# Optimization experiments

Hardware: AMD Instinct MI355X
Metric: run time of the kernel (lower is better)

The kernel has to match this reference:

```python
import jax, jax.numpy as jnp
import numpy as np

TS = 1.0  # simulation time step (Ts from network.yaml)


def alpha_psp(x, tau):
    """SLAYER psp: causal temporal conv of x (time-major, (T,...)) with the
    SRM alpha kernel eps[k] = (k*Ts/tau)*exp(1 - k*Ts/tau), scaled by Ts.
    eps[k] = (Ts*e/tau) * k * d**k with d = exp(-Ts/tau), realized exactly by a
    2-state linear recurrence instead of an O(T^2) FIR."""
    d = jnp.asarray(np.exp(-TS / tau), x.dtype)
    c = jnp.asarray(np.e * TS / tau * TS, x.dtype)  # kernel amp * Ts integration

    def step(carry, x_t):
        u, v = carry                       # u = sum x_s d^(t-1-s); v = sum x_s (t-1-s) d^(t-1-s)
        v_new = d * (v + u)                # -> sum_{s<=t} x_s (t-s) d^(t-s)  (x_t weight 0)
        u_new = d * u + x_t
        return (u_new, v_new), c * v_new

    z = jnp.zeros_like(x[0])
    _, out = jax.lax.scan(step, (z, z), x)
    return out


def lif_spike(u_in, theta, tauRef, scaleRef):
    """SLAYER spike function: sequential threshold over time with alpha-shaped
    refractory response nu[k] = -scaleRef*theta*(k*Ts/tauRef)*exp(1-k*Ts/tauRef)
    added after every spike. Same 2-state recurrence generates the refractory
    sum exactly. u_in is time-major (T, ...). Spike amplitude is 1/Ts."""
    d = jnp.asarray(np.exp(-TS / tauRef), u_in.dtype)
    c = jnp.asarray(-scaleRef * theta * np.e * TS / tauRef, u_in.dtype)

    def step(carry, u_t):
        u, v = carry
        v_new = d * (v + u)                # refractory state from past spikes only
        m = u_t + c * v_new                # membrane potential incl. refractory
        s = (m >= theta).astype(u_t.dtype)
        return (d * u + s, v_new), (s / TS, m)

    z = jnp.zeros_like(u_in[0])
    _, (spikes, membrane) = jax.lax.scan(step, (z, z), u_in)
    return spikes, membrane


def conv2d_t(x, w, pad):
    """Per-time-step 2D conv (SLAYER conv3d with time-kernel 1, no bias).
    x: (T, N, C, H, W), w: (O, I, kh, kw)."""
    T, N, C, H, W = x.shape
    y = jax.lax.conv_general_dilated(
        x.reshape(T * N, C, H, W), w, (1, 1), [(pad, pad), (pad, pad)],
        dimension_numbers=('NCHW', 'OIHW', 'NCHW'))
    return y.reshape(T, N, -1, H, W)


def setup_inputs() -> dict:
    key = jax.random.key(0)
    k1, k2, k3 = jax.random.split(key, 3)
    # binary event spike train, (N, C, H, W, T)
    spikeInput = (jax.random.uniform(k1, (4, 1, 192, 192, 64)) < 0.2).astype(jnp.float32)
    # SLAYER conv weights (bias=False); scaled up (weightScale~100 in SLAYER)
    W1 = jax.random.normal(k2, (1, 1, 5, 5), jnp.float32) * 10.0
    W2 = jax.random.normal(k3, (1, 1, 3, 3), jnp.float32) * 10.0
    return {"spikeInput": spikeInput, "W1": W1, "W2": W2}


def reference(spikeInput, W1, W2):
    x = jnp.moveaxis(spikeInput, -1, 0)          # (T, N, C, H, W) time-major
    psp1 = alpha_psp(x, tau=1.0)                 # slayer1.psp (tauSr=1)
    s1, _ = lif_spike(conv2d_t(psp1, W1, 2), theta=30.0, tauRef=1.0, scaleRef=1.0)
    psp2 = alpha_psp(s1, tau=2.0)                # slayer2.psp (tauSr=2)
    s2, _ = lif_spike(conv2d_t(psp2, W2, 1), theta=50.0, tauRef=2.0, scaleRef=1.0)
    return jnp.moveaxis(s2, 0, -1)               # back to (N, C, H, W, T)
```

## Files before the change

### kernel.cpp

```cpp
#include <hip/hip_runtime.h>


#define HH   192
#define WW   192
#define NIMG 4
#define TT   64
#define TILE 16
#define NT   256
#define XW   6
#define XH   12

#define E_D 2.718281828459045
static constexpr float D1  = (float)0.36787944117144233;
static constexpr float CP1 = (float)(E_D);
static constexpr float DR1 = (float)0.36787944117144233;
static constexpr float CR1 = (float)(-30.0 * E_D);
static constexpr float D2  = (float)0.6065306597126334;
static constexpr float CP2 = (float)(E_D * 0.5);
static constexpr float DR2 = (float)0.6065306597126334;
static constexpr float CR2 = (float)(-50.0 * E_D * 0.5);
static constexpr float TH1 = 30.0f;
static constexpr float TH2 = 50.0f;

__global__ __launch_bounds__(NT)
void ka_pack(const float* __restrict__ in, unsigned* __restrict__ bitT) {
    const int gw = blockIdx.x * (NT / 64) + (threadIdx.x >> 6);
    const int ln = threadIdx.x & 63;
    const int xw = gw % XW;
    const int ny = gw / XW;
    const float* src = in + ((size_t)ny * WW + xw * 32) * TT + ln;
    unsigned w = 0u;
#pragma unroll
    for (int x = 0; x < 32; x++) {
        const float v = src[(size_t)x * TT];
        w |= (v != 0.f) ? (1u << x) : 0u;
    }
    bitT[((size_t)ny * XW + xw) * TT + ln] = w;
}

__global__ __launch_bounds__(NT, 1)
void kb_layer1(const unsigned* __restrict__ bitT, const float* __restrict__ w1g,
               unsigned short* __restrict__ s1h) {
    __shared__ __align__(16) float ct[NT * 65];
    __shared__ float lut[5 * 32];

    const int n = blockIdx.z, ty = blockIdx.y, tx = blockIdx.x;
    const int y0 = ty * TILE, x0 = tx * TILE;
    const int tid = threadIdx.x;
    const int wv = tid >> 6, ln = tid & 63;

    if (tid < 160) {
        const int r = tid >> 5, p = tid & 31;
        float s = 0.f;
#pragma unroll
        for (int j = 0; j < 5; j++)
            if ((p >> j) & 1) s += w1g[r * 5 + j];
        lut[tid] = s;
    }

    const int a = (x0 - 2) >> 5;
    const int s = (x0 - 2) & 31;
    unsigned w20[8];
#pragma unroll
    for (int rr = 0; rr < 8; rr++) {
        const int gy = y0 - 2 + wv * 4 + rr;
        unsigned wa = 0u, wb = 0u;
        if (gy >= 0 && gy < HH) {
            const unsigned* rp = bitT + ((size_t)(n * HH + gy) * XW) * TT + ln;
            if (a >= 0)     wa = rp[(size_t)a * TT];
            if (a + 1 < XW) wb = rp[(size_t)(a + 1) * TT];
        }
        w20[rr] = (wa >> s) | (wb << (32 - s));
    }
    __syncthreads();

#pragma unroll
    for (int rp = 0; rp < 4; rp++) {
        const int row = wv * 4 + rp;
#pragma unroll
        for (int col = 0; col < 16; col++) {
            const float c =
                ((lut[  0 + ((w20[rp + 0] >> col) & 31)]
                + lut[ 32 + ((w20[rp + 1] >> col) & 31)])
                + (lut[ 64 + ((w20[rp + 2] >> col) & 31)]
                +  lut[ 96 + ((w20[rp + 3] >> col) & 31)]))
                +  lut[128 + ((w20[rp + 4] >> col) & 31)];
            ct[(row * 16 + col) * 65 + ln] = c;
        }
    }
    __syncthreads();

    unsigned slo = 0u, shi = 0u;
    {
        const int px = tid;
        float u1 = 0.f, v1 = 0.f, ur = 0.f, vr = 0.f;
#pragma unroll
        for (int tc = 0; tc < TT; tc += 8) {
            float c8[8];
#pragma unroll
            for (int j = 0; j < 8; j++) c8[j] = ct[px * 65 + tc + j];
#pragma unroll
            for (int j = 0; j < 8; j++) {
                v1 = D1 * (v1 + u1);
                const float p = CP1 * v1;
                u1 = D1 * u1 + c8[j];
                vr = DR1 * (vr + ur);
                const float m = p + CR1 * vr;
                const bool sp = (m >= TH1);
                ur = DR1 * ur + (sp ? 1.f : 0.f);
                const unsigned bit = sp ? (1u << ((tc + j) & 31)) : 0u;
                if (tc < 32) slo |= bit;
                else         shi |= bit;
            }
        }
    }
    __syncthreads();
    ((uint2*)ct)[tid] = make_uint2(slo, shi);
    __syncthreads();

    const uint2* tb = (const uint2*)ct;
#pragma unroll
    for (int rp = 0; rp < 4; rp++) {
        const int yl = wv * 4 + rp;
        unsigned h = 0u;
#pragma unroll
        for (int x = 0; x < 16; x++) {
            const uint2 b = tb[yl * 16 + x];
            const unsigned w = (ln < 32) ? b.x : b.y;
            h |= ((w >> (ln & 31)) & 1u) << x;
        }
        s1h[((size_t)(n * HH + y0 + yl) * XH + tx) * TT + ln] = (unsigned short)h;
    }
}

__global__ __launch_bounds__(NT, 1)
void kc_layer2(const unsigned short* __restrict__ s1h, const float* __restrict__ w2g,
               float* __restrict__ out) {
    __shared__ __align__(16) float ct[NT * 65];
    __shared__ float lut[3 * 8];

    const int n = blockIdx.z, ty = blockIdx.y, tx = blockIdx.x;
    const int y0 = ty * TILE, x0 = tx * TILE;
    const int tid = threadIdx.x;
    const int wv = tid >> 6, ln = tid & 63;

    if (tid < 24) {
        const int r = tid >> 3, p = tid & 7;
        float s = 0.f;
#pragma unroll
        for (int j = 0; j < 3; j++)
            if ((p >> j) & 1) s += w2g[r * 3 + j];
        lut[tid] = s;
    }

    unsigned w18[6];
#pragma unroll
    for (int rr = 0; rr < 6; rr++) {
        const int gy = y0 - 1 + wv * 4 + rr;
        unsigned hm = 0u, h0 = 0u, hp = 0u;
        if (gy >= 0 && gy < HH) {
            const unsigned short* rp = s1h + ((size_t)(n * HH + gy) * XH) * TT + ln;
            if (tx > 0)      hm = rp[(size_t)(tx - 1) * TT];
            h0 = rp[(size_t)tx * TT];
            if (tx + 1 < XH) hp = rp[(size_t)(tx + 1) * TT];
        }
        w18[rr] = (hm >> 15) | (h0 << 1) | ((hp & 1u) << 17);
    }
    __syncthreads();

#pragma unroll
    for (int rp = 0; rp < 4; rp++) {
        const int row = wv * 4 + rp;
#pragma unroll
        for (int col = 0; col < 16; col++) {
            const float c =
                (lut[ 0 + ((w18[rp + 0] >> col) & 7)]
               + lut[ 8 + ((w18[rp + 1] >> col) & 7)])
               + lut[16 + ((w18[rp + 2] >> col) & 7)];
            ct[(row * 16 + col) * 65 + ln] = c;
        }
    }
    __syncthreads();

    unsigned olo = 0u, ohi = 0u;
    {
        const int px = tid;
        float u2 = 0.f, v2 = 0.f, ur2 = 0.f, vr2 = 0.f;
#pragma unroll
        for (int tc = 0; tc < TT; tc += 8) {
            float c8[8];
#pragma unroll
            for (int j = 0; j < 8; j++) c8[j] = ct[px * 65 + tc + j];
#pragma unroll
            for (int j = 0; j < 8; j++) {
                v2 = D2 * (v2 + u2);
                const float p = CP2 * v2;
                u2 = D2 * u2 + c8[j];
                vr2 = DR2 * (vr2 + ur2);
                const float m = p + CR2 * vr2;
                const bool sp = (m >= TH2);
                ur2 = DR2 * ur2 + (sp ? 1.f : 0.f);
                const unsigned bit = sp ? (1u << ((tc + j) & 31)) : 0u;
                if (tc < 32) olo |= bit;
                else         ohi |= bit;
            }
        }
    }
    __syncthreads();
    ((uint2*)ct)[tid] = make_uint2(olo, ohi);
    __syncthreads();

    const uint2* tb = (const uint2*)ct;
    const int sh = ln & 31;
#pragma unroll
    for (int k = 0; k < 64; k++) {
        const int p = wv * 64 + k;
        const uint2 b = tb[p];
        const unsigned w = (ln < 32) ? b.x : b.y;
        out[((size_t)(n * HH + y0 + (p >> 4)) * WW + x0 + (p & 15)) * TT + ln] =
            (float)((w >> sh) & 1u);
    }
}

extern "C" void kernel_launch(void* const* d_in, const int* in_sizes, int n_in,
                              void* d_out, int out_size, void* d_ws, size_t ws_size,
                              hipStream_t stream) {
    const float* in = (const float*)d_in[0];
    const float* w1 = (const float*)d_in[1];
    const float* w2 = (const float*)d_in[2];
    float* out = (float*)d_out;

    char* ws = (char*)d_ws;
    unsigned*       bitT = (unsigned*)ws;
    unsigned short* s1h  = (unsigned short*)(ws + (2u << 20));

    const int ka_blocks = (NIMG * HH * XW) / (NT / 64);
    dim3 tgrid(WW / TILE, HH / TILE, NIMG);
    ka_pack  <<<ka_blocks, NT, 0, stream>>>(in, bitT);
    kb_layer1<<<tgrid, NT, 0, stream>>>(bitT, w1, s1h);
    kc_layer2<<<tgrid, NT, 0, stream>>>(s1h, w2, out);
}
```

Measured before the change: 124.9 us.

## Split fused layer kernels into separate conv and scan kernels via global staging

Splits each fused layer kernel into a convolution kernel that writes per-pixel time series to global memory and a scan kernel that reads them back with vector loads. This drops the large shared-memory transpose buffer, so occupancy can rise. Layer 2 now stores 9-bit neighbourhood patterns and looks them up in a 512-entry table, and the output is written as contiguous float4 per pixel. The cost is about 38MB of extra global write and read traffic for the layer-1 float staging, plus two more kernel launches.

```diff
diff --git a/kernel.cpp b/kernel.cpp
--- a/kernel.cpp
+++ b/kernel.cpp
@@ -5,10 +5,10 @@
 #define WW   192
 #define NIMG 4
 #define TT   64
-#define TILE 16
 #define NT   256
 #define XW   6
 #define XH   12
+#define SPR  12
 
 #define E_D 2.718281828459045
 static constexpr float D1  = (float)0.36787944117144233;
@@ -38,16 +38,13 @@
     bitT[((size_t)ny * XW + xw) * TT + ln] = w;
 }
 
-__global__ __launch_bounds__(NT, 1)
-void kb_layer1(const unsigned* __restrict__ bitT, const float* __restrict__ w1g,
-               unsigned short* __restrict__ s1h) {
-    __shared__ __align__(16) float ct[NT * 65];
+__global__ __launch_bounds__(NT)
+void k1_conv1(const unsigned* __restrict__ bitT, const float* __restrict__ w1g,
+              float* __restrict__ ct1) {
     __shared__ float lut[5 * 32];
-
-    const int n = blockIdx.z, ty = blockIdx.y, tx = blockIdx.x;
-    const int y0 = ty * TILE, x0 = tx * TILE;
+    const int n = blockIdx.z, gy = blockIdx.y * 4 + (threadIdx.x >> 6);
+    const int xs = blockIdx.x, ln = threadIdx.x & 63;
     const int tid = threadIdx.x;
-    const int wv = tid >> 6, ln = tid & 63;
 
     if (tid < 160) {
         const int r = tid >> 5, p = tid & 31;
@@ -58,67 +55,75 @@
         lut[tid] = s;
     }
 
+    const int x0 = xs * 16;
     const int a = (x0 - 2) >> 5;
     const int s = (x0 - 2) & 31;
-    unsigned w20[8];
-#pragma unroll
-    for (int rr = 0; rr < 8; rr++) {
-        const int gy = y0 - 2 + wv * 4 + rr;
+    unsigned w20[5];
+#pragma unroll
+    for (int dy = 0; dy < 5; dy++) {
+        const int yy = gy - 2 + dy;
         unsigned wa = 0u, wb = 0u;
-        if (gy >= 0 && gy < HH) {
-            const unsigned* rp = bitT + ((size_t)(n * HH + gy) * XW) * TT + ln;
+        if (yy >= 0 && yy < HH) {
+            const unsigned* rp = bitT + ((size_t)(n * HH + yy) * XW) * TT + ln;
             if (a >= 0)     wa = rp[(size_t)a * TT];
             if (a + 1 < XW) wb = rp[(size_t)(a + 1) * TT];
         }
-        w20[rr] = (wa >> s) | (wb << (32 - s));
+        w20[dy] = (wa >> s) | (wb << (32 - s));
     }
     __syncthreads();
 
-#pragma unroll
-    for (int rp = 0; rp < 4; rp++) {
-        const int row = wv * 4 + rp;
-#pragma unroll
-        for (int col = 0; col < 16; col++) {
-            const float c =
-                ((lut[  0 + ((w20[rp + 0] >> col) & 31)]
-                + lut[ 32 + ((w20[rp + 1] >> col) & 31)])
-                + (lut[ 64 + ((w20[rp + 2] >> col) & 31)]
-                +  lut[ 96 + ((w20[rp + 3] >> col) & 31)]))
-                +  lut[128 + ((w20[rp + 4] >> col) & 31)];
-            ct[(row * 16 + col) * 65 + ln] = c;
-        }
-    }
+    float* op = ct1 + ((size_t)(n * HH + gy) * SPR + xs) * 16 * TT + ln;
+#pragma unroll
+    for (int col = 0; col < 16; col++) {
+        const float c =
+            ((lut[  0 + ((w20[0] >> col) & 31)]
+            + lut[ 32 + ((w20[1] >> col) & 31)])
+            + (lut[ 64 + ((w20[2] >> col) & 31)]
+            +  lut[ 96 + ((w20[3] >> col) & 31)]))
+            +  lut[128 + ((w20[4] >> col) & 31)];
+        op[(size_t)col * TT] = c;
+    }
+}
+
+__global__ __launch_bounds__(NT, 1)
+void k2_scan1(const float* __restrict__ ct1, unsigned short* __restrict__ s1h) {
+    __shared__ uint2 tb[NT];
+    const int n = blockIdx.z, by = blockIdx.y, bx = blockIdx.x;
+    const int tid = threadIdx.x;
+    const int y = by * 16 + (tid >> 4);
+
+    const float4* p = reinterpret_cast<const float4*>(
+        ct1 + (((size_t)(n * HH + y) * SPR + bx) * 16 + (tid & 15)) * TT);
+    float c[TT];
+#pragma unroll
+    for (int j = 0; j < 16; j++) {
+        const float4 v = p[j];
+        c[4 * j + 0] = v.x; c[4 * j + 1] = v.y;
+        c[4 * j + 2] = v.z; c[4 * j + 3] = v.w;
+    }
+
+    float u1 = 0.f, v1 = 0.f, ur = 0.f, vr = 0.f;
+    unsigned slo = 0u, shi = 0u;
+#pragma unroll
+    for (int tc = 0; tc < TT; tc += 8) {
+#pragma unroll
+        for (int j = 0; j < 8; j++) {
+            v1 = D1 * (v1 + u1);
+            const float pp = CP1 * v1;
+            u1 = D1 * u1 + c[tc + j];
+            vr = DR1 * (vr + ur);
+            const float m = pp + CR1 * vr;
+            const bool sp = (m >= TH1);
+            ur = DR1 * ur + (sp ? 1.f : 0.f);
+            const unsigned bit = sp ? (1u << ((tc + j) & 31)) : 0u;
+            if (tc < 32) slo |= bit;
+            else         shi |= bit;
+        }
+    }
+    tb[tid] = make_uint2(slo, shi);
     __syncthreads();
 
-    unsigned slo = 0u, shi = 0u;
-    {
-        const int px = tid;
-        float u1 = 0.f, v1 = 0.f, ur = 0.f, vr = 0.f;
-#pragma unroll
-        for (int tc = 0; tc < TT; tc += 8) {
-            float c8[8];
-#pragma unroll
-            for (int j = 0; j < 8; j++) c8[j] = ct[px * 65 + tc + j];
-#pragma unroll
-            for (int j = 0; j < 8; j++) {
-                v1 = D1 * (v1 + u1);
-                const float p = CP1 * v1;
-                u1 = D1 * u1 + c8[j];
-                vr = DR1 * (vr + ur);
-                const float m = p + CR1 * vr;
-                const bool sp = (m >= TH1);
-                ur = DR1 * ur + (sp ? 1.f : 0.f);
-                const unsigned bit = sp ? (1u << ((tc + j) & 31)) : 0u;
-                if (tc < 32) slo |= bit;
-                else         shi |= bit;
-            }
-        }
-    }
-    __syncthreads();
-    ((uint2*)ct)[tid] = make_uint2(slo, shi);
-    __syncthreads();
-
-    const uint2* tb = (const uint2*)ct;
+    const int wv = tid >> 6, ln = tid & 63;
 #pragma unroll
     for (int rp = 0; rp < 4; rp++) {
         const int yl = wv * 4 + rp;
@@ -129,96 +134,111 @@
             const unsigned w = (ln < 32) ? b.x : b.y;
             h |= ((w >> (ln & 31)) & 1u) << x;
         }
-        s1h[((size_t)(n * HH + y0 + yl) * XH + tx) * TT + ln] = (unsigned short)h;
-    }
-}
-
-__global__ __launch_bounds__(NT, 1)
-void kc_layer2(const unsigned short* __restrict__ s1h, const float* __restrict__ w2g,
-               float* __restrict__ out) {
-    __shared__ __align__(16) float ct[NT * 65];
-    __shared__ float lut[3 * 8];
-
-    const int n = blockIdx.z, ty = blockIdx.y, tx = blockIdx.x;
-    const int y0 = ty * TILE, x0 = tx * TILE;
-    const int tid = threadIdx.x;
-    const int wv = tid >> 6, ln = tid & 63;
-
-    if (tid < 24) {
-        const int r = tid >> 3, p = tid & 7;
-        float s = 0.f;
-#pragma unroll
-        for (int j = 0; j < 3; j++)
-            if ((p >> j) & 1) s += w2g[r * 3 + j];
-        lut[tid] = s;
-    }
-
-    unsigned w18[6];
-#pragma unroll
-    for (int rr = 0; rr < 6; rr++) {
-        const int gy = y0 - 1 + wv * 4 + rr;
+        s1h[((size_t)(n * HH + by * 16 + yl) * XH + bx) * TT + ln] =
+            (unsigned short)h;
+    }
+}
+
+__global__ __launch_bounds__(NT)
+void k3_conv2(const unsigned short* __restrict__ s1h,
+              unsigned short* __restrict__ ct2p) {
+    const int n = blockIdx.z, gy = blockIdx.y * 4 + (threadIdx.x >> 6);
+    const int tx = blockIdx.x, ln = threadIdx.x & 63;
+
+    unsigned w18[3];
+#pragma unroll
+    for (int dy = 0; dy < 3; dy++) {
+        const int yy = gy - 1 + dy;
         unsigned hm = 0u, h0 = 0u, hp = 0u;
-        if (gy >= 0 && gy < HH) {
-            const unsigned short* rp = s1h + ((size_t)(n * HH + gy) * XH) * TT + ln;
+        if (yy >= 0 && yy < HH) {
+            const unsigned short* rp =
+                s1h + ((size_t)(n * HH + yy) * XH) * TT + ln;
             if (tx > 0)      hm = rp[(size_t)(tx - 1) * TT];
             h0 = rp[(size_t)tx * TT];
             if (tx + 1 < XH) hp = rp[(size_t)(tx + 1) * TT];
         }
-        w18[rr] = (hm >> 15) | (h0 << 1) | ((hp & 1u) << 17);
+        w18[dy] = (hm >> 15) | (h0 << 1) | ((hp & 1u) << 17);
+    }
+
+    unsigned short* op =
+        ct2p + ((size_t)(n * HH + gy) * SPR + tx) * 16 * TT + ln;
+#pragma unroll
+    for (int col = 0; col < 16; col++) {
+        const unsigned pat = ((w18[0] >> col) & 7)
+                           | (((w18[1] >> col) & 7) << 3)
+                           | (((w18[2] >> col) & 7) << 6);
+        op[(size_t)col * TT] = (unsigned short)pat;
+    }
+}
+
+__global__ __launch_bounds__(NT, 1)
+void k4_scan2(const unsigned short* __restrict__ ct2p,
+              const float* __restrict__ w2g, float* __restrict__ out) {
+    __shared__ float lut3[512];
+    const int n = blockIdx.z, by = blockIdx.y, bx = blockIdx.x;
+    const int tid = threadIdx.x;
+
+#pragma unroll
+    for (int e = tid; e < 512; e += NT) {
+        float l0 = 0.f, l1 = 0.f, l2 = 0.f;
+#pragma unroll
+        for (int j = 0; j < 3; j++) {
+            if ((e >> j) & 1)       l0 += w2g[j];
+            if ((e >> (3 + j)) & 1) l1 += w2g[3 + j];
+            if ((e >> (6 + j)) & 1) l2 += w2g[6 + j];
+        }
+        lut3[e] = (l0 + l1) + l2;
     }
     __syncthreads();
 
-#pragma unroll
-    for (int rp = 0; rp < 4; rp++) {
-        const int row = wv * 4 + rp;
-#pragma unroll
-        for (int col = 0; col < 16; col++) {
-            const float c =
-                (lut[ 0 + ((w18[rp + 0] >> col) & 7)]
-               + lut[ 8 + ((w18[rp + 1] >> col) & 7)])
-               + lut[16 + ((w18[rp + 2] >> col) & 7)];
-            ct[(row * 16 + col) * 65 + ln] = c;
-        }
-    }
-    __syncthreads();
-
+    const int y = by * 16 + (tid >> 4), x = bx * 16 + (tid & 15);
+    const uint4* pp = reinterpret_cast<const uint4*>(
+        ct2p + (((size_t)(n * HH + y) * SPR + bx) * 16 + (tid & 15)) * TT);
+    uint4 pr[8];
+#pragma unroll
+    for (int j = 0; j < 8; j++) pr[j] = pp[j];
+
+    float l[TT];
+#pragma unroll
+    for (int j = 0; j < 8; j++) {
+        const unsigned q[4] = {pr[j].x, pr[j].y, pr[j].z, pr[j].w};
+#pragma unroll
+        for (int h = 0; h < 4; h++) {
+            l[j * 8 + 2 * h + 0] = lut3[q[h] & 0x1ffu];
+            l[j * 8 + 2 * h + 1] = lut3[(q[h] >> 16) & 0x1ffu];
+        }
+    }
+
+    float u2 = 0.f, v2 = 0.f, ur2 = 0.f, vr2 = 0.f;
     unsigned olo = 0u, ohi = 0u;
-    {
-        const int px = tid;
-        float u2 = 0.f, v2 = 0.f, ur2 = 0.f, vr2 = 0.f;
-#pragma unroll
-        for (int tc = 0; tc < TT; tc += 8) {
-            float c8[8];
-#pragma unroll
-            for (int j = 0; j < 8; j++) c8[j] = ct[px * 65 + tc + j];
-#pragma unroll
-            for (int j = 0; j < 8; j++) {
-                v2 = D2 * (v2 + u2);
-                const float p = CP2 * v2;
-                u2 = D2 * u2 + c8[j];
-                vr2 = DR2 * (vr2 + ur2);
-                const float m = p + CR2 * vr2;
-                const bool sp = (m >= TH2);
-                ur2 = DR2 * ur2 + (sp ? 1.f : 0.f);
-                const unsigned bit = sp ? (1u << ((tc + j) & 31)) : 0u;
-                if (tc < 32) olo |= bit;
-                else         ohi |= bit;
-            }
-        }
-    }
-    __syncthreads();
-    ((uint2*)ct)[tid] = make_uint2(olo, ohi);
-    __syncthreads();
-
-    const uint2* tb = (const uint2*)ct;
-    const int sh = ln & 31;
-#pragma unroll
-    for (int k = 0; k < 64; k++) {
-        const int p = wv * 64 + k;
-        const uint2 b = tb[p];
-        const unsigned w = (ln < 32) ? b.x : b.y;
-        out[((size_t)(n * HH + y0 + (p >> 4)) * WW + x0 + (p & 15)) * TT + ln] =
-            (float)((w >> sh) & 1u);
+#pragma unroll
+    for (int tc = 0; tc < TT; tc += 8) {
+#pragma unroll
+        for (int j = 0; j < 8; j++) {
+            v2 = D2 * (v2 + u2);
+            const float p = CP2 * v2;
+            u2 = D2 * u2 + l[tc + j];
+            vr2 = DR2 * (vr2 + ur2);
+            const float m = p + CR2 * vr2;
+            const bool sp = (m >= TH2);
+            ur2 = DR2 * ur2 + (sp ? 1.f : 0.f);
+            const unsigned bit = sp ? (1u << ((tc + j) & 31)) : 0u;
+            if (tc < 32) olo |= bit;
+            else         ohi |= bit;
+        }
+    }
+
+    float* op = out + ((size_t)(n * HH + y) * WW + x) * TT;
+#pragma unroll
+    for (int c = 0; c < 16; c++) {
+        const unsigned word = (c < 8) ? olo : ohi;
+        const int sh = (4 * c) & 31;
+        float4 v;
+        v.x = (float)((word >> (sh + 0)) & 1u);
+        v.y = (float)((word >> (sh + 1)) & 1u);
+        v.z = (float)((word >> (sh + 2)) & 1u);
+        v.w = (float)((word >> (sh + 3)) & 1u);
+        reinterpret_cast<float4*>(op)[c] = v;
     }
 }
 
@@ -232,11 +252,16 @@
 
     char* ws = (char*)d_ws;
     unsigned*       bitT = (unsigned*)ws;
-    unsigned short* s1h  = (unsigned short*)(ws + (2u << 20));
+    unsigned short* s1h  = (unsigned short*)(ws + (2ull << 20));
+    float*          ct1  = (float*)(ws + (4ull << 20));
+    unsigned short* ct2p = (unsigned short*)(ws + (44ull << 20));
 
     const int ka_blocks = (NIMG * HH * XW) / (NT / 64);
-    dim3 tgrid(WW / TILE, HH / TILE, NIMG);
-    ka_pack  <<<ka_blocks, NT, 0, stream>>>(in, bitT);
-    kb_layer1<<<tgrid, NT, 0, stream>>>(bitT, w1, s1h);
-    kc_layer2<<<tgrid, NT, 0, stream>>>(s1h, w2, out);
-}
+    dim3 cgrid(SPR, HH / 4, NIMG);
+    dim3 sgrid(SPR, HH / 16, NIMG);
+    ka_pack <<<ka_blocks, NT, 0, stream>>>(in, bitT);
+    k1_conv1<<<cgrid, NT, 0, stream>>>(bitT, w1, ct1);
+    k2_scan1<<<sgrid, NT, 0, stream>>>(ct1, s1h);
+    k3_conv2<<<cgrid, NT, 0, stream>>>(s1h, ct2p);
+    k4_scan2<<<sgrid, NT, 0, stream>>>(ct2p, w2, out);
+}
```

Measured after the change: 137.1 us. 1.1x slower.
